# Optimization experiments

Measured on AMD Instinct MI355X. Metric: run time of the kernel, lower is better.

Reference implementation:

```python
import jax, jax.numpy as jnp
import numpy as np

# config (matches init_kwargs)
SEAS = 24      # seasonality
IS = 24        # input_size
OS = 48        # output_size
LVP = 80       # level_variability_penalty (>0 -> compute mean_sq_log_diff)
B = 1024       # batch of series in this forward call
T = 2048       # training timesteps per series
C = 6          # info_cat width
NS = 4096      # num_series (parameter table rows)


def setup_inputs() -> dict:
    key = jax.random.key(0)
    k1, k2, k3, k4, k5 = jax.random.split(key, 5)
    train = jax.random.uniform(k1, (B, T), dtype=jnp.float32, minval=0.5, maxval=1.5)
    val = jax.random.uniform(k2, (B, OS), dtype=jnp.float32, minval=0.5, maxval=1.5)
    test = jax.random.uniform(k3, (B, OS), dtype=jnp.float32, minval=0.5, maxval=1.5)
    info_cat = jax.random.uniform(k4, (B, C), dtype=jnp.float32)
    idxs = jax.random.randint(k5, (B,), 0, NS)
    # learned per-series parameters (torch initializes all to 0.5)
    init_lev_sms = jnp.full((NS,), 0.5, dtype=jnp.float32)
    init_seas_sms = jnp.full((NS,), 0.5, dtype=jnp.float32)
    init_seasonalities = jnp.full((NS, SEAS), 0.5, dtype=jnp.float32)
    return {
        "train": train, "val": val, "test": test, "info_cat": info_cat,
        "init_lev_sms": init_lev_sms, "init_seas_sms": init_seas_sms,
        "init_seasonalities": init_seasonalities, "idxs": idxs,
    }


def reference(train, val, test, info_cat, init_lev_sms, init_seas_sms,
              init_seasonalities, idxs):
    # testing=False -> val/test unused. add_nl_layer path never reached in source.
    x = train.astype(jnp.float32)                       # [B, T]
    Tn = x.shape[1]
    lev_a = jax.nn.sigmoid(init_lev_sms[idxs])          # [B] level smoothing
    seas_b = jax.nn.sigmoid(init_seas_sms[idxs])        # [B] seasonality smoothing
    seas0 = jnp.exp(init_seasonalities[idxs])           # [B, SEAS] initial seasonalities

    lev0 = x[:, 0] / seas0[:, 0]                        # [B]

    # Seasonality produced at step i is consumed at step i+SEAS, so a circular
    # buffer of size SEAS suffices. The torch list's extra element s[SEAS] equals
    # s[0], which is exactly what buffer slot 0 still holds at step i=SEAS.
    def step(carry, inp):
        prev_lev, buf = carry                           # prev_lev [B], buf [B, SEAS]
        xi, pos = inp
        s_i = buf[:, pos]                               # seasonalities[i]
        new_lev = lev_a * (xi / s_i) + (1.0 - lev_a) * prev_lev
        log_diff = jnp.log(new_lev / prev_lev)
        new_seas = seas_b * (xi / new_lev) + (1.0 - seas_b) * s_i
        buf = buf.at[:, pos].set(new_seas)
        return (new_lev, buf), (new_lev, new_seas, log_diff)

    pos_seq = jnp.arange(1, Tn) % SEAS
    (_, _), (levs_seq, seas_seq, ld_seq) = jax.lax.scan(
        step, (lev0, seas0), (x[:, 1:].T, pos_seq))

    levs = jnp.concatenate([lev0[:, None], levs_seq.T], axis=1)          # [B, T]
    # order: initial SEAS values, duplicate of s[0], then per-step appends
    seas_full = jnp.concatenate([seas0, seas0[:, 0:1], seas_seq.T], axis=1)  # [B, T+SEAS]

    # level variability penalty term (LVP > 0)
    d = ld_seq[1:] - ld_seq[:-1]                                         # [T-2, B]
    mean_sq_log_diff = jnp.mean(d * d, axis=1)                           # [T-2]

    if OS > SEAS:  # static config branch: extend seasonality by its last SEAS cols
        seas_full = jnp.concatenate([seas_full, seas_full[:, -SEAS:]], axis=1)

    deseas = x / seas_full[:, :Tn]                                       # [B, T]
    W = Tn - OS - IS + 1                                                 # num windows
    cols = jnp.arange(W)[:, None] + jnp.arange(IS)[None, :]              # [W, IS]
    win = deseas[:, cols]                                                # [B, W, IS]
    normed = win / levs[:, IS - 1: IS - 1 + W][:, :, None]               # [B, W, IS]
    wb = jnp.transpose(normed, (1, 0, 2))                                # [W, B, IS]
    ic = jnp.broadcast_to(info_cat[None], (W, B, C))
    input_batch = jnp.concatenate([wb, ic], axis=2)                      # [W, B, IS+C]

    return input_batch, levs, seas_full, mean_sq_log_diff
```

## Files before the change

### kernel.cpp

```cpp
#include <hip/hip_runtime.h>

#define B_    1024
#define T_    2048
#define SEAS_ 24
#define C_    6
#define W_    1977
#define SFW_  2096
#define NCH_  17
#define WT_   32
#define BT_   8
#define NWT_  62
#define NBT_  128
#define NWIN_ (NWT_ * NBT_)

typedef float vf2 __attribute__((ext_vector_type(2)));
typedef float vf4 __attribute__((ext_vector_type(4)));

__device__ __forceinline__ float frcp(float x) { return __builtin_amdgcn_rcpf(x); }
__device__ __forceinline__ float getc(const float4& v, int c) {
    return c == 0 ? v.x : c == 1 ? v.y : c == 2 ? v.z : v.w;
}

template <int CTRL>
__device__ __forceinline__ float dpp_z(float v) {
    return __int_as_float(__builtin_amdgcn_update_dpp(
        0, __float_as_int(v), CTRL, 0xf, 0xf, true));
}
__device__ __forceinline__ float dpp_bcast15_z(float v) {
    return __int_as_float(__builtin_amdgcn_update_dpp(
        0, __float_as_int(v), 0x142, 0xa, 0xf, false));
}
__device__ __forceinline__ float readlane_f(float v, int l) {
    return __int_as_float(__builtin_amdgcn_readlane(__float_as_int(v), l));
}

__device__ __forceinline__ void scan_block(
    float xv, float& s_own, float& lev, float lev_a, float seas_b, float omb,
    float p1, float p2, float p4, float p8, float wrow, float myp)
{
    float ar  = lev_a * (xv * frcp(s_own));
    float acc = ar;
    acc = __builtin_fmaf(p1, dpp_z<0x111>(acc), acc);
    acc = __builtin_fmaf(p2, dpp_z<0x112>(acc), acc);
    acc = __builtin_fmaf(p4, dpp_z<0x114>(acc), acc);
    acc = __builtin_fmaf(p8, dpp_z<0x118>(acc), acc);
    acc = __builtin_fmaf(wrow, dpp_bcast15_z(acc), acc);
    float lv = __builtin_fmaf(myp, lev, acc);
    float ns = __builtin_fmaf(omb, s_own, seas_b * (xv * frcp(lv)));
    s_own = ns;
    lev = readlane_f(lv, 23);
}

__global__ __launch_bounds__(64, 1) void scan_phase1(
    const float* __restrict__ x, const float* __restrict__ lev_sms,
    const float* __restrict__ seas_sms, const float* __restrict__ seasonalities,
    const int* __restrict__ idxs, float* __restrict__ state)
{
    int b    = blockIdx.x;
    int lane = threadIdx.x;
    const float* xr = x + (size_t)b * T_;

    int id = idxs[b];
    float lev_a  = 1.0f / (1.0f + __expf(-lev_sms[id]));
    float seas_b = 1.0f / (1.0f + __expf(-seas_sms[id]));
    float oma = 1.0f - lev_a, omb = 1.0f - seas_b;

    float p1 = oma, p2 = p1 * p1, p4 = p2 * p2, p8 = p4 * p4, p16 = p8 * p8;
    int lp1 = lane + 1;
    float myp = ((lp1 & 1)  ? p1  : 1.0f) * ((lp1 & 2)  ? p2  : 1.0f)
              * ((lp1 & 4)  ? p4  : 1.0f) * ((lp1 & 8)  ? p8  : 1.0f)
              * ((lp1 & 16) ? p16 : 1.0f);
    int e = lane - 15;
    float wrow = 0.0f;
    if (e > 0) {
        wrow = ((e & 1) ? p1 : 1.0f) * ((e & 2) ? p2 : 1.0f)
             * ((e & 4) ? p4 : 1.0f) * ((e & 8) ? p8 : 1.0f);
    }

    int pos_own = (lane + 1 < 24) ? (lane + 1) : 0;
    float s_own = 1.0f;
    if (lane < 24) s_own = __expf(seasonalities[id * SEAS_ + pos_own]);

    float s0  = readlane_f(s_own, 23);
    float lev = xr[0] * frcp(s0);

    float xA0 = xr[1 +   0 + lane], xA1 = xr[1 +  24 + lane], xA2 = xr[1 +  48 + lane],
          xA3 = xr[1 +  72 + lane], xA4 = xr[1 +  96 + lane];
    float xB0 = xr[1 + 120 + lane], xB1 = xr[1 + 144 + lane], xB2 = xr[1 + 168 + lane],
          xB3 = xr[1 + 192 + lane], xB4 = xr[1 + 216 + lane];

    for (int g = 0; g < 16; g += 2) {
        int baseA = 1 + 5 * (g + 2) * 24 + lane;
        scan_block(xA0, s_own, lev, lev_a, seas_b, omb, p1, p2, p4, p8, wrow, myp);
        { int t = baseA;      xA0 = xr[t > 2047 ? 2047 : t]; }
        scan_block(xA1, s_own, lev, lev_a, seas_b, omb, p1, p2, p4, p8, wrow, myp);
        { int t = baseA + 24; xA1 = xr[t > 2047 ? 2047 : t]; }
        scan_block(xA2, s_own, lev, lev_a, seas_b, omb, p1, p2, p4, p8, wrow, myp);
        { int t = baseA + 48; xA2 = xr[t > 2047 ? 2047 : t]; }
        scan_block(xA3, s_own, lev, lev_a, seas_b, omb, p1, p2, p4, p8, wrow, myp);
        { int t = baseA + 72; xA3 = xr[t > 2047 ? 2047 : t]; }
        scan_block(xA4, s_own, lev, lev_a, seas_b, omb, p1, p2, p4, p8, wrow, myp);
        { int t = baseA + 96; xA4 = xr[t > 2047 ? 2047 : t]; }
        {   float* st = state + ((size_t)g * B_ + b) * 25;
            if (lane < 24) st[pos_own] = s_own;
            if (lane == 24) st[24] = lev;
        }
        int baseB = 1 + 5 * (g + 3) * 24 + lane;
        scan_block(xB0, s_own, lev, lev_a, seas_b, omb, p1, p2, p4, p8, wrow, myp);
        { int t = baseB;      xB0 = xr[t > 2047 ? 2047 : t]; }
        scan_block(xB1, s_own, lev, lev_a, seas_b, omb, p1, p2, p4, p8, wrow, myp);
        { int t = baseB + 24; xB1 = xr[t > 2047 ? 2047 : t]; }
        scan_block(xB2, s_own, lev, lev_a, seas_b, omb, p1, p2, p4, p8, wrow, myp);
        { int t = baseB + 48; xB2 = xr[t > 2047 ? 2047 : t]; }
        scan_block(xB3, s_own, lev, lev_a, seas_b, omb, p1, p2, p4, p8, wrow, myp);
        { int t = baseB + 72; xB3 = xr[t > 2047 ? 2047 : t]; }
        scan_block(xB4, s_own, lev, lev_a, seas_b, omb, p1, p2, p4, p8, wrow, myp);
        { int t = baseB + 96; xB4 = xr[t > 2047 ? 2047 : t]; }
        {   float* st = state + ((size_t)(g + 1) * B_ + b) * 25;
            if (lane < 24) st[pos_own] = s_own;
            if (lane == 24) st[24] = lev;
        }
    }
}

__device__ __forceinline__ void es_block24_lds(
    const float4* __restrict__ xv, float* __restrict__ s,
    float lev_a, float oma, float seas_b, float omb, float& lev,
    float* __restrict__ levp, float* __restrict__ lrow, float* __restrict__ nrow)
{
    float ar[24], lv[24];
    #pragma unroll
    for (int j = 0; j < 24; ++j) {
        const int e = j + 1, pos = (j + 1 < 24) ? (j + 1) : 0;
        ar[j] = lev_a * (getc(xv[e >> 2], e & 3) * frcp(s[pos]));
    }
    #pragma unroll
    for (int j = 0; j < 24; ++j) {
        lev = __builtin_fmaf(oma, lev, ar[j]);
        lv[j] = lev;
    }
    #pragma unroll
    for (int j = 0; j < 24; ++j) {
        const int e = j + 1, pos = (j + 1 < 24) ? (j + 1) : 0;
        float xi = getc(xv[e >> 2], e & 3);
        float ns = __builtin_fmaf(omb, s[pos], seas_b * (xi * frcp(lv[j])));
        s[pos] = ns;
        levp[(size_t)j * B_] = lv[j];
        lrow[j] = lv[j];
        nrow[j] = ns;
    }
}

__global__ __launch_bounds__(64, 1) void scan_phase2(
    const float* __restrict__ x, const float* __restrict__ lev_sms,
    const float* __restrict__ seas_sms, const float* __restrict__ seasonalities,
    const int* __restrict__ idxs, const float* __restrict__ state,
    float* __restrict__ levT, float* __restrict__ out_levs,
    float* __restrict__ out_seas)
{
    __shared__ float lev_lds[64][129];
    __shared__ float ns_lds[64][129];
    int tid = threadIdx.x;
    int b = blockIdx.x * 64 + tid;
    int c = blockIdx.y;
    const float4* xr4 = (const float4*)(x + (size_t)b * T_);

    int id = idxs[b];
    float lev_a  = 1.0f / (1.0f + __expf(-lev_sms[id]));
    float seas_b = 1.0f / (1.0f + __expf(-seas_sms[id]));
    float oma = 1.0f - lev_a, omb = 1.0f - seas_b;

    float s[SEAS_];
    float lev;
    if (c == 0) {
        #pragma unroll
        for (int j = 0; j < SEAS_; ++j) s[j] = __expf(seasonalities[id * SEAS_ + j]);
        #pragma unroll
        for (int j = 0; j < SEAS_; ++j) ns_lds[tid][j] = s[j];
        ns_lds[tid][24] = s[0];
        __syncthreads();
        for (int r = 0; r < 64; ++r) {
            int bb = blockIdx.x * 64 + r;
            if (tid < 25) out_seas[(size_t)bb * SFW_ + tid] = ns_lds[r][tid];
        }
        __syncthreads();
        lev = getc(xr4[0], 0) * frcp(s[0]);
        levT[b] = lev;
        out_levs[(size_t)b * T_] = lev;
    } else {
        const float* st = state + ((size_t)(c - 1) * B_ + b) * 25;
        #pragma unroll
        for (int j = 0; j < SEAS_; ++j) s[j] = st[j];
        lev = st[24];
    }

    float4 xv[7], xn[7];
    const float4* base0 = xr4 + 30 * c;
    #pragma unroll
    for (int q = 0; q < 7; ++q) xv[q] = base0[q];

    float* levp = levT + (size_t)(120 * c + 1) * B_ + b;

    #pragma unroll
    for (int kb = 0; kb < 5; ++kb) {
        const float4* nb = xr4 + 30 * c + 6 * (kb + 1);
        if (c == NCH_ - 1 && kb == 4) {
            xn[0] = nb[0]; xn[1] = nb[1];
        } else {
            #pragma unroll
            for (int q = 0; q < 7; ++q) xn[q] = nb[q];
        }
        es_block24_lds(xv, s, lev_a, oma, seas_b, omb, lev, levp,
                       &lev_lds[tid][kb * 24], &ns_lds[tid][kb * 24]);
        levp += (size_t)24 * B_;
        #pragma unroll
        for (int q = 0; q < 7; ++q) xv[q] = xn[q];
    }
    if (c == NCH_ - 1) {
        #pragma unroll
        for (int j = 0; j < 7; ++j) {
            const int e = j + 1, pos = j + 1;
            float xi    = getc(xv[e >> 2], e & 3);
            float ratio = xi * frcp(s[pos]);
            float nl    = __builtin_fmaf(oma, lev, lev_a * ratio);
            float ns    = __builtin_fmaf(omb, s[pos], seas_b * (xi * frcp(nl)));
            s[pos] = ns;
            lev = nl;
            levp[0] = nl;  levp += B_;
            lev_lds[tid][120 + j] = nl;
            ns_lds[tid][120 + j]  = ns;
        }
    }

    __syncthreads();
    int tb = 120 * c + 1;
    int NT = (c == NCH_ - 1) ? 127 : 120;
    for (int r = 0; r < 64; ++r) {
        int bb = blockIdx.x * 64 + r;
        float* ol = out_levs + (size_t)bb * T_ + tb;
        float* os = out_seas + (size_t)bb * SFW_ + tb + 24;
        ol[tid] = lev_lds[r][tid];
        os[tid] = ns_lds[r][tid];
        int t2 = tid + 64;
        if (t2 < NT) {
            ol[t2] = lev_lds[r][t2];
            os[t2] = ns_lds[r][t2];
        }
        if (c == NCH_ - 1 && tid < 24)
            out_seas[(size_t)bb * SFW_ + 2072 + tid] = ns_lds[r][103 + tid];
    }
}

__global__ __launch_bounds__(256) void mega_kernel(
    const float* __restrict__ x, const float* __restrict__ levs,
    const float* __restrict__ seasF, const float* __restrict__ info_cat,
    const float* __restrict__ levT, vf4* __restrict__ out4,
    float* __restrict__ out_msld)
{
    int bid = blockIdx.x;
    int tid = threadIdx.x;
    if (bid < NWIN_) {
        __shared__ float x_t[BT_][57];
        __shared__ float s_t[BT_][57];
        __shared__ float l_t[BT_][33];
        __shared__ float ic[BT_][8];
        __shared__ __align__(16) vf2 ob[WT_][120];

        int wt = bid / NBT_;
        int bt = bid - wt * NBT_;
        int w0 = wt * WT_;
        int b0 = bt * BT_;

        if (tid < 112) {
            int b = tid / 14, q = tid - b * 14;
            vf4 v = ((const vf4*)(x + (size_t)(b0 + b) * T_ + w0))[q];
            x_t[b][4 * q + 0] = v.x; x_t[b][4 * q + 1] = v.y;
            x_t[b][4 * q + 2] = v.z; x_t[b][4 * q + 3] = v.w;
        } else if (tid < 224) {
            int t2 = tid - 112;
            int b = t2 / 14, q = t2 - b * 14;
            vf4 v = ((const vf4*)(seasF + (size_t)(b0 + b) * SFW_ + w0))[q];
            s_t[b][4 * q + 0] = v.x; s_t[b][4 * q + 1] = v.y;
            s_t[b][4 * q + 2] = v.z; s_t[b][4 * q + 3] = v.w;
        }
        {
            int b = tid >> 5, w = tid & 31;
            l_t[b][w] = levs[(size_t)(b0 + b) * T_ + w0 + w + 23];
        }
        if (tid < 48) {
            int b = tid / 6, cc = tid - b * 6;
            ic[b][cc] = info_cat[(b0 + b) * C_ + cc];
        }
        __syncthreads();

        int w_l = tid >> 3, b_l = tid & 7;
        if (w0 + w_l < W_) {
            float inv = frcp(l_t[b_l][w_l]);
            vf2* obr = &ob[w_l][b_l * 15];
            #pragma unroll
            for (int j = 0; j < 12; ++j) {
                int t = w_l + 2 * j;
                vf2 v;
                v.x = x_t[b_l][t]     * frcp(s_t[b_l][t])     * inv;
                v.y = x_t[b_l][t + 1] * frcp(s_t[b_l][t + 1]) * inv;
                obr[j] = v;
            }
            #pragma unroll
            for (int j = 12; j < 15; ++j) {
                int cc = 2 * (j - 12);
                vf2 v;
                v.x = ic[b_l][cc];
                v.y = ic[b_l][cc + 1];
                obr[j] = v;
            }
        }
        __syncthreads();

        const vf4* obf4 = (const vf4*)ob;
        #pragma unroll
        for (int k = 0; k < 8; ++k) {
            int g = tid + k * 256;
            if (g < 1920) {
                int w_l2 = g / 60, q = g - w_l2 * 60;
                if (w0 + w_l2 < W_) {
                    __builtin_nontemporal_store(
                        obf4[g], &out4[(size_t)(w0 + w_l2) * 7680 + bt * 60 + q]);
                }
            }
        }
    } else {
        int i = bid - NWIN_;
        const float* r0 = levT + (size_t)i * B_;
        float ssum = 0.0f;
        #pragma unroll
        for (int r = 0; r < 4; ++r) {
            int b = tid + 256 * r;
            float l0 = __logf(r0[b]);
            float l1 = __logf(r0[b + B_]);
            float l2 = __logf(r0[b + 2 * B_]);
            float d  = l2 - 2.0f * l1 + l0;
            ssum = __builtin_fmaf(d, d, ssum);
        }
        #pragma unroll
        for (int off = 32; off > 0; off >>= 1) ssum += __shfl_down(ssum, off);
        __shared__ float partial[4];
        int wid = tid >> 6;
        if ((tid & 63) == 0) partial[wid] = ssum;
        __syncthreads();
        if (tid == 0)
            out_msld[i] = (partial[0] + partial[1] + partial[2] + partial[3])
                          * (1.0f / 1024.0f);
    }
}

extern "C" void kernel_launch(void* const* d_in, const int* in_sizes, int n_in,
                              void* d_out, int out_size, void* d_ws, size_t ws_size,
                              hipStream_t stream)
{
    const float* train    = (const float*)d_in[0];
    const float* info_cat = (const float*)d_in[3];
    const float* lev_sms  = (const float*)d_in[4];
    const float* seas_sms = (const float*)d_in[5];
    const float* seasonal = (const float*)d_in[6];
    const int*   idxs     = (const int*)d_in[7];

    float* out      = (float*)d_out;
    float* out_ib   = out;
    float* out_levs = out + (size_t)W_ * B_ * 30;
    float* out_seas = out_levs + (size_t)B_ * T_;
    float* out_msld = out_seas + (size_t)B_ * SFW_;

    float* ws   = (float*)d_ws;
    float* levT = ws;

    float* state = out_ib;

    scan_phase1<<<B_, 64, 0, stream>>>(train, lev_sms, seas_sms, seasonal, idxs, state);

    scan_phase2<<<dim3(B_ / 64, NCH_), 64, 0, stream>>>(train, lev_sms, seas_sms,
                                                        seasonal, idxs, state,
                                                        levT, out_levs, out_seas);

    mega_kernel<<<NWIN_ + 2046, 256, 0, stream>>>(
        train, out_levs, out_seas, info_cat, levT, (vf4*)out_ib, out_msld);
}
```

Before: 81.59 us.

## Shrink scan chunk size from 120 to 48 steps to parallelize phase 2

The two-phase ES scan now checkpoints state every 48 timesteps instead of every 120, giving 43 chunks rather than 17. Phase 1 writes more checkpoints with a shorter unroll. Phase 2 launches more blocks, each with a shorter serial recurrence and smaller LDS staging. The aim is to cut the serial critical path and raise occupancy in phase 2, at the cost of more state traffic and narrower, less coalesced writeback rows.

```diff
diff --git a/kernel.cpp b/kernel.cpp
--- a/kernel.cpp
+++ b/kernel.cpp
@@ -6,7 +6,8 @@
 #define C_    6
 #define W_    1977
 #define SFW_  2096
-#define NCH_  17
+#define CH2_  48
+#define NCH_  43
 #define WT_   32
 #define BT_   8
 #define NWT_  62
@@ -84,39 +85,25 @@
     float s0  = readlane_f(s_own, 23);
     float lev = xr[0] * frcp(s0);
 
-    float xA0 = xr[1 +   0 + lane], xA1 = xr[1 +  24 + lane], xA2 = xr[1 +  48 + lane],
-          xA3 = xr[1 +  72 + lane], xA4 = xr[1 +  96 + lane];
-    float xB0 = xr[1 + 120 + lane], xB1 = xr[1 + 144 + lane], xB2 = xr[1 + 168 + lane],
-          xB3 = xr[1 + 192 + lane], xB4 = xr[1 + 216 + lane];
-
-    for (int g = 0; g < 16; g += 2) {
-        int baseA = 1 + 5 * (g + 2) * 24 + lane;
+    float xA0 = xr[1 +  0 + lane], xA1 = xr[1 + 24 + lane];
+    float xB0 = xr[1 + 48 + lane], xB1 = xr[1 + 72 + lane];
+
+    for (int p = 0; p < 21; ++p) {
+        int baseA = 1 + (4 * p + 4) * 24 + lane;
         scan_block(xA0, s_own, lev, lev_a, seas_b, omb, p1, p2, p4, p8, wrow, myp);
         { int t = baseA;      xA0 = xr[t > 2047 ? 2047 : t]; }
         scan_block(xA1, s_own, lev, lev_a, seas_b, omb, p1, p2, p4, p8, wrow, myp);
         { int t = baseA + 24; xA1 = xr[t > 2047 ? 2047 : t]; }
-        scan_block(xA2, s_own, lev, lev_a, seas_b, omb, p1, p2, p4, p8, wrow, myp);
-        { int t = baseA + 48; xA2 = xr[t > 2047 ? 2047 : t]; }
-        scan_block(xA3, s_own, lev, lev_a, seas_b, omb, p1, p2, p4, p8, wrow, myp);
-        { int t = baseA + 72; xA3 = xr[t > 2047 ? 2047 : t]; }
-        scan_block(xA4, s_own, lev, lev_a, seas_b, omb, p1, p2, p4, p8, wrow, myp);
-        { int t = baseA + 96; xA4 = xr[t > 2047 ? 2047 : t]; }
-        {   float* st = state + ((size_t)g * B_ + b) * 25;
+        {   float* st = state + ((size_t)(2 * p) * B_ + b) * 25;
             if (lane < 24) st[pos_own] = s_own;
             if (lane == 24) st[24] = lev;
         }
-        int baseB = 1 + 5 * (g + 3) * 24 + lane;
+        int baseB = 1 + (4 * p + 6) * 24 + lane;
         scan_block(xB0, s_own, lev, lev_a, seas_b, omb, p1, p2, p4, p8, wrow, myp);
         { int t = baseB;      xB0 = xr[t > 2047 ? 2047 : t]; }
         scan_block(xB1, s_own, lev, lev_a, seas_b, omb, p1, p2, p4, p8, wrow, myp);
         { int t = baseB + 24; xB1 = xr[t > 2047 ? 2047 : t]; }
-        scan_block(xB2, s_own, lev, lev_a, seas_b, omb, p1, p2, p4, p8, wrow, myp);
-        { int t = baseB + 48; xB2 = xr[t > 2047 ? 2047 : t]; }
-        scan_block(xB3, s_own, lev, lev_a, seas_b, omb, p1, p2, p4, p8, wrow, myp);
-        { int t = baseB + 72; xB3 = xr[t > 2047 ? 2047 : t]; }
-        scan_block(xB4, s_own, lev, lev_a, seas_b, omb, p1, p2, p4, p8, wrow, myp);
-        { int t = baseB + 96; xB4 = xr[t > 2047 ? 2047 : t]; }
-        {   float* st = state + ((size_t)(g + 1) * B_ + b) * 25;
+        {   float* st = state + ((size_t)(2 * p + 1) * B_ + b) * 25;
             if (lane < 24) st[pos_own] = s_own;
             if (lane == 24) st[24] = lev;
         }
@@ -158,8 +145,8 @@
     float* __restrict__ levT, float* __restrict__ out_levs,
     float* __restrict__ out_seas)
 {
-    __shared__ float lev_lds[64][129];
-    __shared__ float ns_lds[64][129];
+    __shared__ float lev_lds[64][57];
+    __shared__ float ns_lds[64][57];
     int tid = threadIdx.x;
     int b = blockIdx.x * 64 + tid;
     int c = blockIdx.y;
@@ -195,28 +182,28 @@
     }
 
     float4 xv[7], xn[7];
-    const float4* base0 = xr4 + 30 * c;
+    const float4* base0 = xr4 + 12 * c;
     #pragma unroll
     for (int q = 0; q < 7; ++q) xv[q] = base0[q];
 
-    float* levp = levT + (size_t)(120 * c + 1) * B_ + b;
-
-    #pragma unroll
-    for (int kb = 0; kb < 5; ++kb) {
-        const float4* nb = xr4 + 30 * c + 6 * (kb + 1);
-        if (c == NCH_ - 1 && kb == 4) {
-            xn[0] = nb[0]; xn[1] = nb[1];
-        } else {
-            #pragma unroll
-            for (int q = 0; q < 7; ++q) xn[q] = nb[q];
-        }
+    float* levp = levT + (size_t)(48 * c + 1) * B_ + b;
+
+    if (c == NCH_ - 1) {
+        xn[0] = base0[6]; xn[1] = base0[7];
+    } else {
+        #pragma unroll
+        for (int q = 0; q < 7; ++q) xn[q] = (base0 + 6)[q];
+    }
+    es_block24_lds(xv, s, lev_a, oma, seas_b, omb, lev, levp,
+                   &lev_lds[tid][1], &ns_lds[tid][1]);
+    levp += (size_t)24 * B_;
+    #pragma unroll
+    for (int q = 0; q < 7; ++q) xv[q] = xn[q];
+
+    if (c < NCH_ - 1) {
         es_block24_lds(xv, s, lev_a, oma, seas_b, omb, lev, levp,
-                       &lev_lds[tid][kb * 24], &ns_lds[tid][kb * 24]);
-        levp += (size_t)24 * B_;
-        #pragma unroll
-        for (int q = 0; q < 7; ++q) xv[q] = xn[q];
-    }
-    if (c == NCH_ - 1) {
+                       &lev_lds[tid][25], &ns_lds[tid][25]);
+    } else {
         #pragma unroll
         for (int j = 0; j < 7; ++j) {
             const int e = j + 1, pos = j + 1;
@@ -227,27 +214,22 @@
             s[pos] = ns;
             lev = nl;
             levp[0] = nl;  levp += B_;
-            lev_lds[tid][120 + j] = nl;
-            ns_lds[tid][120 + j]  = ns;
+            lev_lds[tid][25 + j] = nl;
+            ns_lds[tid][25 + j]  = ns;
         }
     }
 
     __syncthreads();
-    int tb = 120 * c + 1;
-    int NT = (c == NCH_ - 1) ? 127 : 120;
+    int tb = 48 * c + 1;
+    int NT = (c == NCH_ - 1) ? 31 : 48;
     for (int r = 0; r < 64; ++r) {
         int bb = blockIdx.x * 64 + r;
-        float* ol = out_levs + (size_t)bb * T_ + tb;
-        float* os = out_seas + (size_t)bb * SFW_ + tb + 24;
-        ol[tid] = lev_lds[r][tid];
-        os[tid] = ns_lds[r][tid];
-        int t2 = tid + 64;
-        if (t2 < NT) {
-            ol[t2] = lev_lds[r][t2];
-            os[t2] = ns_lds[r][t2];
+        if (tid < NT) {
+            out_levs[(size_t)bb * T_ + tb + tid]        = lev_lds[r][1 + tid];
+            out_seas[(size_t)bb * SFW_ + tb + 24 + tid] = ns_lds[r][1 + tid];
         }
         if (c == NCH_ - 1 && tid < 24)
-            out_seas[(size_t)bb * SFW_ + 2072 + tid] = ns_lds[r][103 + tid];
+            out_seas[(size_t)bb * SFW_ + 2072 + tid] = ns_lds[r][8 + tid];
     }
 }
 
```

After: 87.71 us. 1.08x slower.
